# Kernel tuning notes

Hardware: AMD Instinct MI355X
Metric: run time of the kernel (lower is better)

Reference implementation:

```python
import jax, jax.numpy as jnp
import numpy as np

PSIZE = 3
PSTRIDE = 3
N = PSIZE * PSTRIDE   # 9 patches per image
P = PSIZE * PSIZE     # 9 tokens per patch


def setup_inputs() -> dict:
    key = jax.random.key(0)
    k1, k2, k3 = jax.random.split(key, 3)
    B, C = 2048, 512
    H = W = PSIZE * PSTRIDE  # 9, forced by the patch view
    hidden = C // 2
    x = jax.random.normal(k1, (B, H, W, C), dtype=jnp.float32)
    W_fc = jax.random.normal(k2, (hidden, C), dtype=jnp.float32) * (C ** -0.5)
    b_fc = jax.random.normal(k3, (hidden,), dtype=jnp.float32) * 0.01
    return {"x": x, "W_fc": W_fc, "b_fc": b_fc}


def reference(x, W_fc, b_fc):
    B, H, Wd, C = x.shape
    hidden = W_fc.shape[0]
    scale = (hidden * P) ** -0.5
    # partition into N overlapping-free patches: [B, N, P, C]
    xv = x.reshape(B, PSTRIDE, PSIZE, PSTRIDE, PSIZE, C).transpose(0, 1, 3, 2, 4, 5)
    x_fc = xv.reshape(B, N, P, C)
    # fc projection then flatten patch tokens into a per-patch query vector
    xq = (jnp.einsum('bnpc,hc->bnph', x_fc, W_fc) + b_fc).reshape(B, N, P * hidden)
    attn = jnp.einsum('bnd,bmd->bnm', xq, xq) * scale  # [B, N, N]
    # diagonal self-suppression mask (block_idx=0, match_vec=None path)
    mask = jnp.where(jnp.eye(N, dtype=bool), -100.0, 0.0).astype(attn.dtype)
    attn = attn + mask
    # second-order affinity + double softmax
    attn2 = jax.nn.softmax(
        jnp.einsum('bnm,bkm->bnk', attn, attn) * (N ** -0.5), axis=-1)
    attn = jax.nn.softmax(attn + attn2, axis=-1)
    # values are the raw patch pixels flattened: [B, N, P*C]
    v = x_fc.reshape(B, N, P * C)
    x_attn = jnp.einsum('bnm,bmd->bnd', attn, v)
    out = x_attn.reshape(B, PSTRIDE, PSTRIDE, PSIZE, PSIZE, C)
    out = out.transpose(0, 1, 3, 2, 4, 5).reshape(B, H, Wd, C)
    return out
```

## Files before the change

kernel.cpp:

```cpp
#include <hip/hip_runtime.h>

typedef __attribute__((ext_vector_type(8))) short short8;
typedef __attribute__((ext_vector_type(4))) float f32x4;

#define CDIM   512
#define NROWS  81
#define IMG    (NROWS * CDIM)
#define PA     520
#define PQ     264

#define SA_BYTES   (NROWS * PA * 2)
#define SQ_OFFB    84240
#define SQ_BYTES   (NROWS * PQ * 2)
#define SPART_OFFB 127008
#define SATTN_OFFB 135200
#define ST2_OFFB   135584
#define SWGT_OFFB  135968
#define SMEM_BYTES 136352

__device__ __forceinline__ unsigned short f2bf(float f) {
    unsigned int u = __float_as_uint(f);
    u += 0x7fffu + ((u >> 16) & 1u);
    return (unsigned short)(u >> 16);
}
__device__ __forceinline__ float bf2f(unsigned short s) {
    return __uint_as_float(((unsigned int)s) << 16);
}

extern "C" __global__ void __launch_bounds__(512, 1)
attn_kernel(const float* __restrict__ x, const float* __restrict__ Wfc,
            const float* __restrict__ bfc, float* __restrict__ out)
{
    extern __shared__ char smem[];
    unsigned short* sA   = (unsigned short*)(smem);
    unsigned short* sQ   = (unsigned short*)(smem + SQ_OFFB);
    float*          sPart = (float*)(smem + SPART_OFFB);
    float*          sAttn = (float*)(smem + SATTN_OFFB);
    float*          sT2   = (float*)(smem + ST2_OFFB);
    float*          sWgt  = (float*)(smem + SWGT_OFFB);

    const int tid  = threadIdx.x;
    const int wave = tid >> 6;
    const int lane = tid & 63;
    const int r15  = lane & 15;
    const int q    = lane >> 4;
    const long img = blockIdx.x;
    const float* xin = x + img * (long)IMG;

    for (int it = 0; it < 11; ++it) {
        int row = it * 8 + wave;
        if (row < NROWS) {
            int n = row / 9, p = row % 9;
            int h  = (n / 3) * 3 + p / 3;
            int w2 = (n % 3) * 3 + p % 3;
            const float* src = xin + (h * 9 + w2) * CDIM + lane * 8;
            f32x4 v0 = *(const f32x4*)src;
            f32x4 v1 = *(const f32x4*)(src + 4);
            short8 pk;
            pk[0] = (short)f2bf(v0[0]); pk[1] = (short)f2bf(v0[1]);
            pk[2] = (short)f2bf(v0[2]); pk[3] = (short)f2bf(v0[3]);
            pk[4] = (short)f2bf(v1[0]); pk[5] = (short)f2bf(v1[1]);
            pk[6] = (short)f2bf(v1[2]); pk[7] = (short)f2bf(v1[3]);
            *(short8*)&sA[row * PA + lane * 8] = pk;
        }
    }
    __syncthreads();

    f32x4 acc[6][2];
    #pragma unroll
    for (int i = 0; i < 6; ++i) {
        acc[i][0] = (f32x4){0.f, 0.f, 0.f, 0.f};
        acc[i][1] = (f32x4){0.f, 0.f, 0.f, 0.f};
    }
    const float bias0 = bfc[wave * 32 + r15];
    const float bias1 = bfc[wave * 32 + 16 + r15];
    const float* wrow0 = Wfc + (long)(wave * 32 + r15) * CDIM + q * 8;
    const float* wrow1 = wrow0 + 16 * CDIM;

    #pragma unroll 4
    for (int ks = 0; ks < 16; ++ks) {
        const float* s0 = wrow0 + ks * 32;
        const float* s1 = wrow1 + ks * 32;
        f32x4 u0 = *(const f32x4*)s0, u1 = *(const f32x4*)(s0 + 4);
        f32x4 u2 = *(const f32x4*)s1, u3 = *(const f32x4*)(s1 + 4);
        short8 b0, b1;
        b0[0] = (short)f2bf(u0[0]); b0[1] = (short)f2bf(u0[1]);
        b0[2] = (short)f2bf(u0[2]); b0[3] = (short)f2bf(u0[3]);
        b0[4] = (short)f2bf(u1[0]); b0[5] = (short)f2bf(u1[1]);
        b0[6] = (short)f2bf(u1[2]); b0[7] = (short)f2bf(u1[3]);
        b1[0] = (short)f2bf(u2[0]); b1[1] = (short)f2bf(u2[1]);
        b1[2] = (short)f2bf(u2[2]); b1[3] = (short)f2bf(u2[3]);
        b1[4] = (short)f2bf(u3[0]); b1[5] = (short)f2bf(u3[1]);
        b1[6] = (short)f2bf(u3[2]); b1[7] = (short)f2bf(u3[3]);
        #pragma unroll
        for (int mt = 0; mt < 6; ++mt) {
            int rowA = mt * 16 + r15;
            if (rowA > 80) rowA = 80;
            short8 a = *(short8*)&sA[rowA * PA + ks * 32 + q * 8];
            acc[mt][0] = __builtin_amdgcn_mfma_f32_16x16x32_bf16(a, b0, acc[mt][0], 0, 0, 0);
            acc[mt][1] = __builtin_amdgcn_mfma_f32_16x16x32_bf16(a, b1, acc[mt][1], 0, 0, 0);
        }
    }
    #pragma unroll
    for (int mt = 0; mt < 6; ++mt) {
        #pragma unroll
        for (int nt = 0; nt < 2; ++nt) {
            int col = wave * 32 + nt * 16 + r15;
            float bb = nt ? bias1 : bias0;
            #pragma unroll
            for (int r = 0; r < 4; ++r) {
                int row = mt * 16 + q * 4 + r;
                if (row < NROWS)
                    sQ[row * PQ + col] = f2bf(acc[mt][nt][r] + bb);
            }
        }
    }
    __syncthreads();

    f32x4 qacc = (f32x4){0.f, 0.f, 0.f, 0.f};
    for (int p = wave; p < 9; p += 8) {
        int rq = r15 * 9 + p;
        if (rq > 80) rq = 80;
        const unsigned short* qrow = &sQ[rq * PQ + q * 8];
        #pragma unroll
        for (int ks = 0; ks < 8; ++ks) {
            short8 f = *(short8*)&qrow[ks * 32];
            qacc = __builtin_amdgcn_mfma_f32_16x16x32_bf16(f, f, qacc, 0, 0, 0);
        }
    }
    {
        float* pp = &sPart[wave * 256];
        #pragma unroll
        for (int r = 0; r < 4; ++r)
            pp[(q * 4 + r) * 16 + r15] = qacc[r];
    }
    __syncthreads();

    if (tid < 81) {
        int n = tid / 9, m = tid % 9;
        float s = 0.f;
        #pragma unroll
        for (int w = 0; w < 8; ++w) s += sPart[w * 256 + n * 16 + m];
        s *= (1.0f / 48.0f);
        if (n == m) s -= 100.0f;
        sAttn[tid] = s;
    }
    __syncthreads();
    if (tid < 81) {
        int n = tid / 9, k = tid % 9;
        float s = 0.f;
        #pragma unroll
        for (int m = 0; m < 9; ++m) s += sAttn[n * 9 + m] * sAttn[k * 9 + m];
        sT2[tid] = s * (1.0f / 3.0f);
    }
    __syncthreads();
    if (tid < 9) {
        int n = tid;
        float t[9], mx = -1e30f;
        #pragma unroll
        for (int m = 0; m < 9; ++m) { t[m] = sT2[n * 9 + m]; mx = fmaxf(mx, t[m]); }
        float sum = 0.f;
        #pragma unroll
        for (int m = 0; m < 9; ++m) { t[m] = __expf(t[m] - mx); sum += t[m]; }
        float inv = 1.0f / sum;
        float g[9], mx2 = -1e30f;
        #pragma unroll
        for (int m = 0; m < 9; ++m) { g[m] = sAttn[n * 9 + m] + t[m] * inv; mx2 = fmaxf(mx2, g[m]); }
        float sum2 = 0.f;
        #pragma unroll
        for (int m = 0; m < 9; ++m) { g[m] = __expf(g[m] - mx2); sum2 += g[m]; }
        float inv2 = 1.0f / sum2;
        #pragma unroll
        for (int m = 0; m < 9; ++m) sWgt[n * 9 + m] = g[m] * inv2;
    }
    __syncthreads();

    for (int it = 0; it < 11; ++it) {
        int orow = it * 8 + wave;
        if (orow < NROWS) {
            int h = orow / 9, w2 = orow % 9;
            int n = (h / 3) * 3 + w2 / 3;
            int p = (h % 3) * 3 + w2 % 3;
            float av[8] = {0.f, 0.f, 0.f, 0.f, 0.f, 0.f, 0.f, 0.f};
            #pragma unroll
            for (int m = 0; m < 9; ++m) {
                float wt = sWgt[n * 9 + m];
                short8 v = *(short8*)&sA[(m * 9 + p) * PA + lane * 8];
                #pragma unroll
                for (int j = 0; j < 8; ++j)
                    av[j] += wt * bf2f((unsigned short)v[j]);
            }
            float* dst = out + img * (long)IMG + orow * CDIM + lane * 8;
            *(f32x4*)dst       = (f32x4){av[0], av[1], av[2], av[3]};
            *(f32x4*)(dst + 4) = (f32x4){av[4], av[5], av[6], av[7]};
        }
    }
}

extern "C" void kernel_launch(void* const* d_in, const int* in_sizes, int n_in,
                              void* d_out, int out_size, void* d_ws, size_t ws_size,
                              hipStream_t stream) {
    (void)in_sizes; (void)n_in; (void)d_ws; (void)ws_size; (void)out_size;
    const float* x   = (const float*)d_in[0];
    const float* Wfc = (const float*)d_in[1];
    const float* bfc = (const float*)d_in[2];
    float* o = (float*)d_out;
    hipFuncSetAttribute((const void*)attn_kernel,
                        hipFuncAttributeMaxDynamicSharedMemorySize, SMEM_BYTES);
    attn_kernel<<<dim3(2048), dim3(512), SMEM_BYTES, stream>>>(x, Wfc, bfc, o);
}
```

Baseline: 694.9 us.

## Pre-convert weights to bf16, double block to 1024 threads, restructure output accumulation

Adds a small pre-pass kernel that converts W_fc to bf16 once into the workspace, so the main kernel no longer converts weights per block. The main kernel now runs 16 waves per block, splitting the projection GEMM across M and N, splitting the Gram-matrix MFMA work over K halves, and batching the input loads before conversion. The value-weighting stage is reorganized so each wave reads each source patch row once and accumulates all 9 output patches, cutting LDS reads. Shared memory grows for the larger partial-sum buffer, and the larger block raises register pressure.

```diff
diff --git a/kernel.cpp b/kernel.cpp
--- a/kernel.cpp
+++ b/kernel.cpp
@@ -1,6 +1,7 @@
 #include <hip/hip_runtime.h>
 
 typedef __attribute__((ext_vector_type(8))) short short8;
+typedef __attribute__((ext_vector_type(4))) short short4v;
 typedef __attribute__((ext_vector_type(4))) float f32x4;
 
 #define CDIM   512
@@ -13,10 +14,10 @@
 #define SQ_OFFB    84240
 #define SQ_BYTES   (NROWS * PQ * 2)
 #define SPART_OFFB 127008
-#define SATTN_OFFB 135200
-#define ST2_OFFB   135584
-#define SWGT_OFFB  135968
-#define SMEM_BYTES 136352
+#define SATTN_OFFB 143392
+#define ST2_OFFB   143776
+#define SWGT_OFFB  144160
+#define SMEM_BYTES 144544
 
 __device__ __forceinline__ unsigned short f2bf(float f) {
     unsigned int u = __float_as_uint(f);
@@ -27,13 +28,28 @@
     return __uint_as_float(((unsigned int)s) << 16);
 }
 
-extern "C" __global__ void __launch_bounds__(512, 1)
-attn_kernel(const float* __restrict__ x, const float* __restrict__ Wfc,
+extern "C" __global__ void wconv_kernel(const float* __restrict__ Wfc,
+                                        unsigned short* __restrict__ Wbf)
+{
+    const long i = (long)blockIdx.x * 256 + threadIdx.x;
+    const float* src = Wfc + i * 8;
+    f32x4 v0 = *(const f32x4*)src;
+    f32x4 v1 = *(const f32x4*)(src + 4);
+    short8 pk;
+    pk[0] = (short)f2bf(v0[0]); pk[1] = (short)f2bf(v0[1]);
+    pk[2] = (short)f2bf(v0[2]); pk[3] = (short)f2bf(v0[3]);
+    pk[4] = (short)f2bf(v1[0]); pk[5] = (short)f2bf(v1[1]);
+    pk[6] = (short)f2bf(v1[2]); pk[7] = (short)f2bf(v1[3]);
+    *(short8*)(Wbf + i * 8) = pk;
+}
+
+extern "C" __global__ void __launch_bounds__(1024, 4)
+attn_kernel(const float* __restrict__ x, const unsigned short* __restrict__ Wbf,
             const float* __restrict__ bfc, float* __restrict__ out)
 {
     extern __shared__ char smem[];
-    unsigned short* sA   = (unsigned short*)(smem);
-    unsigned short* sQ   = (unsigned short*)(smem + SQ_OFFB);
+    unsigned short* sA    = (unsigned short*)(smem);
+    unsigned short* sQ    = (unsigned short*)(smem + SQ_OFFB);
     float*          sPart = (float*)(smem + SPART_OFFB);
     float*          sAttn = (float*)(smem + SATTN_OFFB);
     float*          sT2   = (float*)(smem + ST2_OFFB);
@@ -47,88 +63,93 @@
     const long img = blockIdx.x;
     const float* xin = x + img * (long)IMG;
 
-    for (int it = 0; it < 11; ++it) {
-        int row = it * 8 + wave;
-        if (row < NROWS) {
-            int n = row / 9, p = row % 9;
-            int h  = (n / 3) * 3 + p / 3;
-            int w2 = (n % 3) * 3 + p % 3;
-            const float* src = xin + (h * 9 + w2) * CDIM + lane * 8;
-            f32x4 v0 = *(const f32x4*)src;
-            f32x4 v1 = *(const f32x4*)(src + 4);
-            short8 pk;
-            pk[0] = (short)f2bf(v0[0]); pk[1] = (short)f2bf(v0[1]);
-            pk[2] = (short)f2bf(v0[2]); pk[3] = (short)f2bf(v0[3]);
-            pk[4] = (short)f2bf(v1[0]); pk[5] = (short)f2bf(v1[1]);
-            pk[6] = (short)f2bf(v1[2]); pk[7] = (short)f2bf(v1[3]);
-            *(short8*)&sA[row * PA + lane * 8] = pk;
-        }
-    }
-    __syncthreads();
-
-    f32x4 acc[6][2];
-    #pragma unroll
-    for (int i = 0; i < 6; ++i) {
-        acc[i][0] = (f32x4){0.f, 0.f, 0.f, 0.f};
-        acc[i][1] = (f32x4){0.f, 0.f, 0.f, 0.f};
-    }
-    const float bias0 = bfc[wave * 32 + r15];
-    const float bias1 = bfc[wave * 32 + 16 + r15];
-    const float* wrow0 = Wfc + (long)(wave * 32 + r15) * CDIM + q * 8;
-    const float* wrow1 = wrow0 + 16 * CDIM;
-
-    #pragma unroll 4
-    for (int ks = 0; ks < 16; ++ks) {
-        const float* s0 = wrow0 + ks * 32;
-        const float* s1 = wrow1 + ks * 32;
-        f32x4 u0 = *(const f32x4*)s0, u1 = *(const f32x4*)(s0 + 4);
-        f32x4 u2 = *(const f32x4*)s1, u3 = *(const f32x4*)(s1 + 4);
-        short8 b0, b1;
-        b0[0] = (short)f2bf(u0[0]); b0[1] = (short)f2bf(u0[1]);
-        b0[2] = (short)f2bf(u0[2]); b0[3] = (short)f2bf(u0[3]);
-        b0[4] = (short)f2bf(u1[0]); b0[5] = (short)f2bf(u1[1]);
-        b0[6] = (short)f2bf(u1[2]); b0[7] = (short)f2bf(u1[3]);
-        b1[0] = (short)f2bf(u2[0]); b1[1] = (short)f2bf(u2[1]);
-        b1[2] = (short)f2bf(u2[2]); b1[3] = (short)f2bf(u2[3]);
-        b1[4] = (short)f2bf(u3[0]); b1[5] = (short)f2bf(u3[1]);
-        b1[6] = (short)f2bf(u3[2]); b1[7] = (short)f2bf(u3[3]);
-        #pragma unroll
-        for (int mt = 0; mt < 6; ++mt) {
-            int rowA = mt * 16 + r15;
-            if (rowA > 80) rowA = 80;
-            short8 a = *(short8*)&sA[rowA * PA + ks * 32 + q * 8];
-            acc[mt][0] = __builtin_amdgcn_mfma_f32_16x16x32_bf16(a, b0, acc[mt][0], 0, 0, 0);
-            acc[mt][1] = __builtin_amdgcn_mfma_f32_16x16x32_bf16(a, b1, acc[mt][1], 0, 0, 0);
-        }
-    }
-    #pragma unroll
-    for (int mt = 0; mt < 6; ++mt) {
-        #pragma unroll
-        for (int nt = 0; nt < 2; ++nt) {
-            int col = wave * 32 + nt * 16 + r15;
-            float bb = nt ? bias1 : bias0;
-            #pragma unroll
-            for (int r = 0; r < 4; ++r) {
-                int row = mt * 16 + q * 4 + r;
-                if (row < NROWS)
-                    sQ[row * PQ + col] = f2bf(acc[mt][nt][r] + bb);
-            }
-        }
-    }
-    __syncthreads();
-
-    f32x4 qacc = (f32x4){0.f, 0.f, 0.f, 0.f};
-    for (int p = wave; p < 9; p += 8) {
-        int rq = r15 * 9 + p;
-        if (rq > 80) rq = 80;
-        const unsigned short* qrow = &sQ[rq * PQ + q * 8];
-        #pragma unroll
-        for (int ks = 0; ks < 8; ++ks) {
-            short8 f = *(short8*)&qrow[ks * 32];
-            qacc = __builtin_amdgcn_mfma_f32_16x16x32_bf16(f, f, qacc, 0, 0, 0);
-        }
-    }
     {
+        f32x4 v0[6], v1[6];
+        #pragma unroll
+        for (int it = 0; it < 6; ++it) {
+            int row = it * 16 + wave;
+            if (row < NROWS) {
+                int n = row / 9, p = row % 9;
+                int h  = (n / 3) * 3 + p / 3;
+                int w2 = (n % 3) * 3 + p % 3;
+                const float* src = xin + (h * 9 + w2) * CDIM + lane * 8;
+                v0[it] = *(const f32x4*)src;
+                v1[it] = *(const f32x4*)(src + 4);
+            }
+        }
+        #pragma unroll
+        for (int it = 0; it < 6; ++it) {
+            int row = it * 16 + wave;
+            if (row < NROWS) {
+                short8 pk;
+                pk[0] = (short)f2bf(v0[it][0]); pk[1] = (short)f2bf(v0[it][1]);
+                pk[2] = (short)f2bf(v0[it][2]); pk[3] = (short)f2bf(v0[it][3]);
+                pk[4] = (short)f2bf(v1[it][0]); pk[5] = (short)f2bf(v1[it][1]);
+                pk[6] = (short)f2bf(v1[it][2]); pk[7] = (short)f2bf(v1[it][3]);
+                *(short8*)&sA[row * PA + lane * 8] = pk;
+            }
+        }
+    }
+    __syncthreads();
+
+    {
+        const int wm = wave >> 3;
+        const int wn = wave & 7;
+        f32x4 acc[3][2];
+        #pragma unroll
+        for (int i = 0; i < 3; ++i) {
+            acc[i][0] = (f32x4){0.f, 0.f, 0.f, 0.f};
+            acc[i][1] = (f32x4){0.f, 0.f, 0.f, 0.f};
+        }
+        const float bias0 = bfc[wn * 32 + r15];
+        const float bias1 = bfc[wn * 32 + 16 + r15];
+        const unsigned short* wr0 = Wbf + (long)(wn * 32 + r15) * CDIM + q * 8;
+        const unsigned short* wr1 = wr0 + 16 * CDIM;
+
+        #pragma unroll 4
+        for (int ks = 0; ks < 16; ++ks) {
+            short8 b0 = *(const short8*)(wr0 + ks * 32);
+            short8 b1 = *(const short8*)(wr1 + ks * 32);
+            #pragma unroll
+            for (int i = 0; i < 3; ++i) {
+                int rowA = (wm * 3 + i) * 16 + r15;
+                if (rowA > 80) rowA = 80;
+                short8 a = *(short8*)&sA[rowA * PA + ks * 32 + q * 8];
+                acc[i][0] = __builtin_amdgcn_mfma_f32_16x16x32_bf16(a, b0, acc[i][0], 0, 0, 0);
+                acc[i][1] = __builtin_amdgcn_mfma_f32_16x16x32_bf16(a, b1, acc[i][1], 0, 0, 0);
+            }
+        }
+        #pragma unroll
+        for (int i = 0; i < 3; ++i) {
+            int mt = wm * 3 + i;
+            #pragma unroll
+            for (int nt = 0; nt < 2; ++nt) {
+                int col = wn * 32 + nt * 16 + r15;
+                float bb = nt ? bias1 : bias0;
+                #pragma unroll
+                for (int r = 0; r < 4; ++r) {
+                    int row = mt * 16 + q * 4 + r;
+                    if (row < NROWS)
+                        sQ[row * PQ + col] = f2bf(acc[i][nt][r] + bb);
+                }
+            }
+        }
+    }
+    __syncthreads();
+
+    {
+        f32x4 qacc = (f32x4){0.f, 0.f, 0.f, 0.f};
+        for (int t = wave; t < 18; t += 16) {
+            int p = t >> 1, kh = t & 1;
+            int rq = r15 * 9 + p;
+            if (rq > 80) rq = 80;
+            const unsigned short* qrow = &sQ[rq * PQ + kh * 128 + q * 8];
+            #pragma unroll
+            for (int ks = 0; ks < 4; ++ks) {
+                short8 f = *(short8*)&qrow[ks * 32];
+                qacc = __builtin_amdgcn_mfma_f32_16x16x32_bf16(f, f, qacc, 0, 0, 0);
+            }
+        }
         float* pp = &sPart[wave * 256];
         #pragma unroll
         for (int r = 0; r < 4; ++r)
@@ -140,7 +161,7 @@
         int n = tid / 9, m = tid % 9;
         float s = 0.f;
         #pragma unroll
-        for (int w = 0; w < 8; ++w) s += sPart[w * 256 + n * 16 + m];
+        for (int w = 0; w < 16; ++w) s += sPart[w * 256 + n * 16 + m];
         s *= (1.0f / 48.0f);
         if (n == m) s -= 100.0f;
         sAttn[tid] = s;
@@ -175,24 +196,32 @@
     }
     __syncthreads();
 
-    for (int it = 0; it < 11; ++it) {
-        int orow = it * 8 + wave;
-        if (orow < NROWS) {
-            int h = orow / 9, w2 = orow % 9;
-            int n = (h / 3) * 3 + w2 / 3;
-            int p = (h % 3) * 3 + w2 % 3;
-            float av[8] = {0.f, 0.f, 0.f, 0.f, 0.f, 0.f, 0.f, 0.f};
-            #pragma unroll
-            for (int m = 0; m < 9; ++m) {
+    for (int t = wave; t < 18; t += 16) {
+        int p = t >> 1, hf = t & 1;
+        int c0 = hf * 256 + lane * 4;
+        f32x4 av[9];
+        #pragma unroll
+        for (int n = 0; n < 9; ++n) av[n] = (f32x4){0.f, 0.f, 0.f, 0.f};
+        #pragma unroll
+        for (int m = 0; m < 9; ++m) {
+            short4v v = *(const short4v*)&sA[(m * 9 + p) * PA + c0];
+            float vf0 = bf2f((unsigned short)v[0]);
+            float vf1 = bf2f((unsigned short)v[1]);
+            float vf2 = bf2f((unsigned short)v[2]);
+            float vf3 = bf2f((unsigned short)v[3]);
+            #pragma unroll
+            for (int n = 0; n < 9; ++n) {
                 float wt = sWgt[n * 9 + m];
-                short8 v = *(short8*)&sA[(m * 9 + p) * PA + lane * 8];
-                #pragma unroll
-                for (int j = 0; j < 8; ++j)
-                    av[j] += wt * bf2f((unsigned short)v[j]);
-            }
-            float* dst = out + img * (long)IMG + orow * CDIM + lane * 8;
-            *(f32x4*)dst       = (f32x4){av[0], av[1], av[2], av[3]};
-            *(f32x4*)(dst + 4) = (f32x4){av[4], av[5], av[6], av[7]};
+                av[n][0] += wt * vf0; av[n][1] += wt * vf1;
+                av[n][2] += wt * vf2; av[n][3] += wt * vf3;
+            }
+        }
+        #pragma unroll
+        for (int n = 0; n < 9; ++n) {
+            int h  = (n / 3) * 3 + p / 3;
+            int w2 = (n % 3) * 3 + p % 3;
+            float* dst = out + img * (long)IMG + (h * 9 + w2) * CDIM + c0;
+            *(f32x4*)dst = av[n];
         }
     }
 }
@@ -200,12 +229,14 @@
 extern "C" void kernel_launch(void* const* d_in, const int* in_sizes, int n_in,
                               void* d_out, int out_size, void* d_ws, size_t ws_size,
                               hipStream_t stream) {
-    (void)in_sizes; (void)n_in; (void)d_ws; (void)ws_size; (void)out_size;
+    (void)in_sizes; (void)n_in; (void)ws_size; (void)out_size;
     const float* x   = (const float*)d_in[0];
     const float* Wfc = (const float*)d_in[1];
     const float* bfc = (const float*)d_in[2];
     float* o = (float*)d_out;
+    unsigned short* Wbf = (unsigned short*)d_ws;
     hipFuncSetAttribute((const void*)attn_kernel,
                         hipFuncAttributeMaxDynamicSharedMemorySize, SMEM_BYTES);
-    attn_kernel<<<dim3(2048), dim3(512), SMEM_BYTES, stream>>>(x, Wfc, bfc, o);
-}
+    wconv_kernel<<<dim3(64), dim3(256), 0, stream>>>(Wfc, Wbf);
+    attn_kernel<<<dim3(2048), dim3(1024), SMEM_BYTES, stream>>>(x, Wbf, bfc, o);
+}
```

After: 927.6 us. +33.5%, slower.
